# Kernel tuning notes

Hardware: AMD Instinct MI355X
Metric: run time of the kernel (lower is better)

Reference implementation:

```python
import jax, jax.numpy as jnp
import numpy as np

T, B, N, H, NT = 4096, 8, 256, 512, 5
W_SCALE = 0.02


def setup_inputs() -> dict:
    key = jax.random.key(0)
    ks = jax.random.split(key, 32)
    f32 = jnp.float32
    d = {}
    d['v_action'] = jax.random.normal(ks[0], (N, B, H), f32)
    d['v_frame'] = jax.random.normal(ks[1], (T, B, H), f32)
    d['v_task'] = jax.random.normal(ks[2], (NT, B, H), f32)
    d['v_mask'] = jax.random.randint(ks[3], (B, N), 0, 2, jnp.int32).at[:, 0].set(1)
    d['t_action'] = jax.random.normal(ks[4], (N, B, H), f32)
    d['t_frame'] = jax.random.normal(ks[5], (T, B, H), f32)
    d['t_task'] = jax.random.normal(ks[6], (NT, B, H), f32)
    d['t_mask'] = jax.random.randint(ks[7], (B, N), 0, 2, jnp.int32).at[:, 0].set(1)
    names = ['v_Wq', 'v_Wk', 'v_Wv', 'v_Wo', 't_Wq', 't_Wk', 't_Wv', 't_Wo']
    for i, nm in enumerate(names):
        d[nm] = jax.random.normal(ks[8 + i], (H, H), f32) * W_SCALE
    d['v_aw'] = jnp.asarray(0.1, f32)
    d['t_aw'] = jnp.asarray(0.1, f32)
    d['v_tw'] = jax.random.normal(ks[20], (H, 1), f32) * W_SCALE
    d['v_tb'] = jnp.zeros((1,), f32)
    d['t_tw'] = jax.random.normal(ks[21], (H, 1), f32) * W_SCALE
    d['t_tb'] = jnp.zeros((1,), f32)
    return d


def _compute_logit(frame, action, Wq, Wk):
    # frame: [T,B,H] queries, action: [N,B,H] keys -> logits [B,T,N]
    q = jnp.einsum('tbf,fh->tbh', frame, Wq)
    k = jnp.einsum('nba,ah->nbh', action, Wk)
    return jnp.einsum('tbh,nbh->btn', q, k) / jnp.sqrt(jnp.asarray(q.shape[-1], q.dtype))


def _compute_output(logit, alignment, action, frame, mask, Wv, Wo, aw):
    # shared detached cross-domain alignment, gated by sigmoid(alignment_weight)
    combined = logit + jax.nn.sigmoid(aw) * alignment          # [B,T,N]
    nomask = combined
    masked = jnp.where(mask[:, None, :] > 0, combined, -jnp.inf)
    attn = jax.nn.softmax(masked, axis=-1)                      # softmax over protos N
    v = jnp.einsum('nba,af->nbf', action, Wv)                   # values from protos
    out = jnp.einsum('btn,nbf->tbf', attn, v)
    out = jnp.einsum('tbf,fg->tbg', out, Wo) + frame            # residual to frames
    return out, nomask


def reference(v_action, v_frame, v_task, v_mask, t_action, t_frame, t_task, t_mask,
              v_Wq, v_Wk, v_Wv, v_Wo, v_aw, v_tw, v_tb,
              t_Wq, t_Wk, t_Wv, t_Wo, t_aw, t_tw, t_tb):
    v_logit = _compute_logit(v_frame, v_action, v_Wq, v_Wk)
    t_logit = _compute_logit(t_frame, t_action, t_Wq, t_Wk)
    v_share = jax.lax.stop_gradient(v_logit)
    t_share = jax.lax.stop_gradient(t_logit)
    v_out, v_nm = _compute_output(v_logit, t_share, v_action, v_frame, v_mask, v_Wv, v_Wo, v_aw)
    t_out, t_nm = _compute_output(t_logit, v_share, t_action, t_frame, t_mask, t_Wv, t_Wo, t_aw)
    v_ta = jnp.einsum('kbh,ho->kbo', v_task, v_tw) + v_tb       # [ntask,B,1]
    t_ta = jnp.einsum('kbh,ho->kbo', t_task, t_tw) + t_tb
    return (v_out, t_out,
            jnp.transpose(v_nm, (0, 2, 1)),                      # [B,N,T]
            jnp.transpose(t_nm, (0, 2, 1)),
            v_ta, t_ta)
```

## Files before the change

### kernel.cpp

```cpp
#include <hip/hip_runtime.h>
#include <hip/hip_bf16.h>
#include <cstddef>
#include <cstdint>

#define T_DIM 4096
#define B_DIM 8
#define N_DIM 256
#define H_DIM 512
#define NT_DIM 5

typedef __attribute__((ext_vector_type(8))) short short8;
typedef __attribute__((ext_vector_type(4))) float f32x4;

__device__ __forceinline__ short cvt_bf16(float f) {
  __hip_bfloat16 h = __float2bfloat16(f);
  union { __hip_bfloat16 h; short s; } u; u.h = h; return u.s;
}
__device__ __forceinline__ float bf2f(short s) {
  union { uint32_t u; float f; } v; v.u = ((uint32_t)(uint16_t)s) << 16;
  return v.f;
}

typedef __attribute__((address_space(1))) const void gvoid_t;
typedef __attribute__((address_space(3))) void lvoid_t;
__device__ __forceinline__ void gl_lds16(const void* g, void* lds_wave_base) {
  __builtin_amdgcn_global_load_lds((gvoid_t*)(uintptr_t)g,
                                   (lvoid_t*)(uint32_t)(uintptr_t)lds_wave_base,
                                   16, 0, 0);
}

#define MFMA16(a, b, c) __builtin_amdgcn_mfma_f32_16x16x32_bf16(a, b, c, 0, 0, 0)

struct GP {
  const void* A[4];
  const short* B[4];
  void* C[4];
  const float* R[4];
  long long a_bs[4], b_bs[4], c_bs[4];
  int lda[4], ldb[4], ldc[4];
  int xlim[4], ylim[4];
};

template<typename TA, typename TC, bool ADD_RES>
__global__ __launch_bounds__(256)
void gemm_tn(GP p, int zlog, int K, float scale) {
  constexpr bool F32A = (sizeof(TA) == 4);
  constexpr int ASTR = F32A ? 40 : 32;
  constexpr int AB = 128 * ASTR * 2;
  constexpr int BB = 128 * 32 * 2;
  constexpr int HALF = AB + BB;
  constexpr int EPIB = 4 * 16 * 68 * 4;
  constexpr int BODYB = F32A ? (2 * AB + 3 * BB) : (3 * HALF);
  constexpr int SMEMB = BODYB > EPIB ? BODYB : EPIB;
  __shared__ __align__(16) char smem[SMEMB];

  const int dom = blockIdx.z >> zlog;
  const long long zz = blockIdx.z & ((1u << zlog) - 1u);
  if ((int)blockIdx.x >= p.xlim[dom] || (int)blockIdx.y >= p.ylim[dom]) return;

  const int lda = p.lda[dom], ldb = p.ldb[dom], ldc = p.ldc[dom];

  const int tid  = threadIdx.x;
  const int lane = tid & 63;
  const int wave = tid >> 6;
  const int wr   = (wave >> 1) * 64;
  const int wc   = (wave & 1) * 64;
  const int lrow = lane & 15;
  const int kgrp = lane >> 4;

  const TA*    Abase = (const TA*)p.A[dom] + zz * p.a_bs[dom] +
                       (long long)(blockIdx.x * 128) * lda;
  const short* Bbase = p.B[dom] + zz * p.b_bs[dom] +
                       (long long)(blockIdx.y * 128) * ldb;

  const int ch_r  = lane >> 2;
  const int swcol = ((lane & 3) ^ (ch_r & 3)) * 8;
  const int srow = tid >> 1;
  const int scol = (tid & 1) * 16;

  f32x4 acc[4][4] = {};
  f32x4 pv[4];

  auto stageA_bf16 = [&](int buf, int k0) {
    short* As = (short*)(smem + buf * HALF);
    #pragma unroll
    for (int i = 0; i < 2; ++i) {
      const int c = wave + 4 * i;
      gl_lds16((const short*)Abase + (long long)(c * 16 + ch_r) * lda + k0 + swcol,
               &As[c * 512]);
    }
  };
  auto stageB_bf16 = [&](int buf, int k0) {
    short* Bs = (short*)(smem + buf * HALF + AB);
    #pragma unroll
    for (int i = 0; i < 2; ++i) {
      const int c = wave + 4 * i;
      gl_lds16(Bbase + (long long)(c * 16 + ch_r) * ldb + k0 + swcol, &Bs[c * 512]);
    }
  };
  auto stageB_f32p = [&](int buf, int k0) {
    short* Bs = (short*)(smem + 2 * AB + buf * BB);
    #pragma unroll
    for (int i = 0; i < 2; ++i) {
      const int c = wave + 4 * i;
      gl_lds16(Bbase + (long long)(c * 16 + ch_r) * ldb + k0 + swcol, &Bs[c * 512]);
    }
  };
  auto loadA_f32 = [&](int k0) {
    const float* gp = (const float*)Abase + (long long)srow * lda + k0 + scol;
    pv[0] = *(const f32x4*)(gp + 0);
    pv[1] = *(const f32x4*)(gp + 4);
    pv[2] = *(const f32x4*)(gp + 8);
    pv[3] = *(const f32x4*)(gp + 12);
  };
  auto writeA_f32 = [&](int buf) {
    short* As = (short*)(smem + buf * AB);
    short8 s0, s1;
    #pragma unroll
    for (int e = 0; e < 4; ++e) {
      s0[e]     = cvt_bf16(pv[0][e]);
      s0[4 + e] = cvt_bf16(pv[1][e]);
      s1[e]     = cvt_bf16(pv[2][e]);
      s1[4 + e] = cvt_bf16(pv[3][e]);
    }
    *(short8*)&As[srow * ASTR + scol]     = s0;
    *(short8*)&As[srow * ASTR + scol + 8] = s1;
  };
  auto compute = [&](int abuf, int bbuf) {
    const short* As = (const short*)(smem + (F32A ? abuf * AB : abuf * HALF));
    const short* Bs = (const short*)(smem + (F32A ? 2 * AB + bbuf * BB
                                                  : bbuf * HALF + AB));
    short8 af[4], bfr[4];
    const int u = kgrp ^ (lrow & 3);
    #pragma unroll
    for (int i = 0; i < 4; ++i) {
      const int row = wr + i * 16 + lrow;
      if constexpr (F32A) af[i] = *(const short8*)&As[row * ASTR + kgrp * 8];
      else                af[i] = *(const short8*)&As[row * 32 + u * 8];
    }
    #pragma unroll
    for (int j = 0; j < 4; ++j) {
      const int row = wc + j * 16 + lrow;
      bfr[j] = *(const short8*)&Bs[row * 32 + u * 8];
    }
    #pragma unroll
    for (int i = 0; i < 4; ++i)
      #pragma unroll
      for (int j = 0; j < 4; ++j)
        acc[i][j] = MFMA16(af[i], bfr[j], acc[i][j]);
  };

  const int NT = K >> 5;
  if constexpr (F32A) {
    loadA_f32(0); writeA_f32(0);
    stageB_f32p(0, 0);
    if (NT > 1) stageB_f32p(1, 32);
    if (NT > 1) loadA_f32(32);
    for (int t = 0; t < NT; ++t) {
      asm volatile("s_waitcnt lgkmcnt(0)" ::: "memory");
      __builtin_amdgcn_sched_barrier(0);
      __builtin_amdgcn_s_barrier();
      if (t + 2 < NT) stageB_f32p((t + 2) % 3, (t + 2) << 5);
      __builtin_amdgcn_sched_barrier(0);
      if (t + 2 < NT)      asm volatile("s_waitcnt vmcnt(8)" ::: "memory");
      else if (t + 1 < NT) asm volatile("s_waitcnt vmcnt(6)" ::: "memory");
      else                 asm volatile("s_waitcnt vmcnt(0)" ::: "memory");
      __builtin_amdgcn_sched_barrier(0);
      __builtin_amdgcn_s_barrier();
      __builtin_amdgcn_sched_barrier(0);
      compute(t & 1, t % 3);
      if (t + 1 < NT) writeA_f32((t + 1) & 1);
      if (t + 2 < NT) loadA_f32((t + 2) << 5);
    }
  } else {
    stageA_bf16(0, 0); stageB_bf16(0, 0);
    if (NT > 1) { stageA_bf16(1, 32); stageB_bf16(1, 32); }
    for (int t = 0; t < NT; ++t) {
      __builtin_amdgcn_s_barrier();
      if (t + 2 < NT) {
        stageA_bf16((t + 2) % 3, (t + 2) << 5);
        stageB_bf16((t + 2) % 3, (t + 2) << 5);
        __builtin_amdgcn_sched_barrier(0);
        asm volatile("s_waitcnt vmcnt(8)" ::: "memory");
      } else if (t + 1 < NT) {
        asm volatile("s_waitcnt vmcnt(4)" ::: "memory");
      } else {
        asm volatile("s_waitcnt vmcnt(0)" ::: "memory");
      }
      __builtin_amdgcn_sched_barrier(0);
      __builtin_amdgcn_s_barrier();
      __builtin_amdgcn_sched_barrier(0);
      compute(t % 3, t % 3);
    }
  }

  __syncthreads();
  float* myEp = (float*)smem + wave * (16 * 68);
  TC* Cd = (TC*)p.C[dom];
  const float* Res = p.R[dom];
  const long long cb = zz * p.c_bs[dom];
  const int gm = blockIdx.x * 128 + wr;
  const int gn = blockIdx.y * 128 + wc;
  const int er = lane >> 2;
  const int ec = (lane & 3) * 16;

  f32x4 resA[4], resB[4];
  if constexpr (ADD_RES) {
    const long long b0 = cb + (long long)(gm + er) * ldc + gn + ec;
    #pragma unroll
    for (int q = 0; q < 4; ++q) resA[q] = *(const f32x4*)&Res[b0 + q * 4];
  }

  #pragma unroll
  for (int i = 0; i < 4; ++i) {
    if constexpr (ADD_RES) {
      if (i < 3) {
        const long long bn = cb + (long long)(gm + (i + 1) * 16 + er) * ldc + gn + ec;
        #pragma unroll
        for (int q = 0; q < 4; ++q) resB[q] = *(const f32x4*)&Res[bn + q * 4];
      }
    }
    #pragma unroll
    for (int j = 0; j < 4; ++j)
      #pragma unroll
      for (int r = 0; r < 4; ++r)
        myEp[(kgrp * 4 + r) * 68 + j * 16 + lrow] = acc[i][j][r];
    float vals[16];
    #pragma unroll
    for (int q = 0; q < 4; ++q) {
      f32x4 t4 = *(const f32x4*)&myEp[er * 68 + ec + q * 4];
      vals[q * 4 + 0] = t4[0]; vals[q * 4 + 1] = t4[1];
      vals[q * 4 + 2] = t4[2]; vals[q * 4 + 3] = t4[3];
    }
    const int row_g = gm + i * 16 + er;
    const long long base = cb + (long long)row_g * ldc + gn + ec;
    if constexpr (sizeof(TC) == 2) {
      short8 s0, s1;
      #pragma unroll
      for (int e = 0; e < 8; ++e) {
        s0[e] = cvt_bf16(vals[e] * scale);
        s1[e] = cvt_bf16(vals[8 + e] * scale);
      }
      *(short8*)&Cd[base]     = s0;
      *(short8*)&Cd[base + 8] = s1;
    } else {
      #pragma unroll
      for (int q = 0; q < 4; ++q) {
        f32x4 o;
        #pragma unroll
        for (int e = 0; e < 4; ++e) o[e] = vals[q * 4 + e] * scale;
        if constexpr (ADD_RES) {
          #pragma unroll
          for (int e = 0; e < 4; ++e) o[e] += resA[q][e];
        }
        *(f32x4*)&Cd[base + q * 4] = o;
      }
    }
    if constexpr (ADD_RES) {
      #pragma unroll
      for (int q = 0; q < 4; ++q) resA[q] = resB[q];
    }
  }
}

struct PrepArgs {
  const float* w6[6];
  const float* w2[2];
  const float* av; const float* at;
  const float* vtask; const float* ttask;
  const float* vtw; const float* vtb;
  const float* ttw; const float* ttb;
  short* WT; short* Ac16v; short* Ac16t;
  float* out_vta; float* out_tta;
};

__global__ __launch_bounds__(256)
void prep_kernel(PrepArgs a) {
  __shared__ float tile[32][33];
  const long long WS = (long long)H_DIM * H_DIM;
  const int bx = blockIdx.x;
  const int tid = threadIdx.x;

  if (bx < 768) {
    const int w = bx >> 7;
    const int blk = bx & 127;
    const float* src = a.w6[w];
    short* d = a.WT + (long long)w * WS;
    const int i = (blk * 256 + tid) * 8;
    f32x4 v0 = *(const f32x4*)(src + i);
    f32x4 v1 = *(const f32x4*)(src + i + 4);
    short8 o;
    #pragma unroll
    for (int e = 0; e < 4; ++e) { o[e] = cvt_bf16(v0[e]); o[4 + e] = cvt_bf16(v1[e]); }
    *(short8*)&d[i] = o;
  } else if (bx < 1280) {
    const int r = bx - 768;
    const int w = r >> 8;
    const int rem = r & 255;
    const int n0 = (rem >> 4) * 32, k0 = (rem & 15) * 32;
    const float* src = a.w2[w];
    short* d = a.WT + (long long)(6 + w) * WS;
    const int tx = tid & 31, ty = tid >> 5;
    #pragma unroll
    for (int i = 0; i < 4; ++i)
      tile[ty + 8 * i][tx] = src[(long long)(k0 + ty + 8 * i) * H_DIM + n0 + tx];
    __syncthreads();
    #pragma unroll
    for (int i = 0; i < 4; ++i)
      d[(long long)(n0 + ty + 8 * i) * H_DIM + k0 + tx] = cvt_bf16(tile[tx][ty + 8 * i]);
  } else if (bx < 2304) {
    const int r = bx - 1280;
    const int dom = r >> 9;
    const int blk = r & 511;
    const float* src = dom ? a.at : a.av;
    short* d = dom ? a.Ac16t : a.Ac16v;
    const int i = (blk * 256 + tid) * 8;
    f32x4 v0 = *(const f32x4*)(src + i);
    f32x4 v1 = *(const f32x4*)(src + i + 4);
    short8 o;
    #pragma unroll
    for (int e = 0; e < 4; ++e) { o[e] = cvt_bf16(v0[e]); o[4 + e] = cvt_bf16(v1[e]); }
    *(short8*)&d[i] = o;
  } else {
    const int wave = tid >> 6;
    const int lane = tid & 63;
    for (int g = wave; g < 16; g += 4) {
      const int dom = g >> 3;
      const int b = g & 7;
      const float* task = dom ? a.ttask : a.vtask;
      const float* tw   = dom ? a.ttw : a.vtw;
      const float  tb   = (dom ? a.ttb : a.vtb)[0];
      float* o = dom ? a.out_tta : a.out_vta;
      for (int k = 0; k < NT_DIM; ++k) {
        const float* row = task + ((long long)k * B_DIM + b) * H_DIM;
        float s = 0.f;
        for (int c = lane; c < H_DIM; c += 64) s += row[c] * tw[c];
        #pragma unroll
        for (int d = 32; d > 0; d >>= 1) s += __shfl_xor(s, d);
        if (lane == 0) o[k * B_DIM + b] = s + tb;
      }
    }
  }
}

__global__ __launch_bounds__(256)
void softmax_fused(const short* __restrict__ Lv, const short* __restrict__ Lt,
                   const int* __restrict__ vmask, const int* __restrict__ tmask,
                   const float* __restrict__ vaw, const float* __restrict__ taw,
                   short* __restrict__ Av, short* __restrict__ At,
                   float* __restrict__ Onm_v, float* __restrict__ Onm_t) {
  __shared__ float tile[16 * 260];
  __shared__ int msk[2][256];
  const int tid = threadIdx.x;
  const int b = blockIdx.y, t0 = blockIdx.x * 16;
  const int r = tid >> 4, seg = tid & 15;
  msk[0][tid] = vmask[b * 256 + tid];
  msk[1][tid] = tmask[b * 256 + tid];
  __syncthreads();
  const float sv = 1.f / (1.f + __expf(-vaw[0]));
  const float st = 1.f / (1.f + __expf(-taw[0]));
  const long long off = ((long long)b * T_DIM + t0 + r) * N_DIM + seg * 16;

  short8 lv0 = *(const short8*)&Lv[off];
  short8 lv1 = *(const short8*)&Lv[off + 8];
  short8 lt0 = *(const short8*)&Lt[off];
  short8 lt1 = *(const short8*)&Lt[off + 8];
  float cv[16], ct[16];
  #pragma unroll
  for (int i = 0; i < 8; ++i) {
    float a0 = bf2f(lv0[i]), b0 = bf2f(lt0[i]);
    float a1 = bf2f(lv1[i]), b1 = bf2f(lt1[i]);
    cv[i]     = a0 + sv * b0;  ct[i]     = b0 + st * a0;
    cv[8 + i] = a1 + sv * b1;  ct[8 + i] = b1 + st * a1;
  }

#define EMIT_DOMAIN(CVAL, DI, AOUT, ONM) do {                                   \
    const int4 mA = *(const int4*)&msk[DI][seg * 16 + 0];                       \
    const int4 mB = *(const int4*)&msk[DI][seg * 16 + 4];                       \
    const int4 mC = *(const int4*)&msk[DI][seg * 16 + 8];                       \
    const int4 mD = *(const int4*)&msk[DI][seg * 16 + 12];                      \
    const int mk[16] = {mA.x, mA.y, mA.z, mA.w, mB.x, mB.y, mB.z, mB.w,         \
                        mC.x, mC.y, mC.z, mC.w, mD.x, mD.y, mD.z, mD.w};        \
    float mx = -3.4e38f;                                                        \
    _Pragma("unroll")                                                           \
    for (int q = 0; q < 16; ++q) if (mk[q] > 0) mx = fmaxf(mx, CVAL[q]);        \
    _Pragma("unroll")                                                           \
    for (int sh = 1; sh < 16; sh <<= 1) mx = fmaxf(mx, __shfl_xor(mx, sh));     \
    float ev[16]; float ssum = 0.f;                                             \
    _Pragma("unroll")                                                           \
    for (int q = 0; q < 16; ++q) {                                              \
      ev[q] = (mk[q] > 0) ? __expf(CVAL[q] - mx) : 0.f; ssum += ev[q];          \
    }                                                                           \
    _Pragma("unroll")                                                           \
    for (int sh = 1; sh < 16; sh <<= 1) ssum += __shfl_xor(ssum, sh);           \
    const float inv = 1.f / ssum;                                               \
    short8 o0, o1;                                                              \
    _Pragma("unroll")                                                           \
    for (int q = 0; q < 8; ++q) {                                               \
      o0[q] = cvt_bf16(ev[q] * inv); o1[q] = cvt_bf16(ev[8 + q] * inv);         \
    }                                                                           \
    *(short8*)&AOUT[off] = o0; *(short8*)&AOUT[off + 8] = o1;                   \
    _Pragma("unroll")                                                           \
    for (int q = 0; q < 4; ++q) {                                               \
      f32x4 tv; tv[0] = CVAL[q * 4]; tv[1] = CVAL[q * 4 + 1];                   \
      tv[2] = CVAL[q * 4 + 2]; tv[3] = CVAL[q * 4 + 3];                         \
      *(f32x4*)&tile[r * 260 + seg * 16 + q * 4] = tv;                          \
    }                                                                           \
    __syncthreads();                                                            \
    {                                                                           \
      float* obase = &ONM[((long long)b * N_DIM + tid) * T_DIM + t0];           \
      _Pragma("unroll")                                                         \
      for (int g = 0; g < 4; ++g) {                                             \
        f32x4 wv;                                                               \
        wv[0] = tile[(4 * g + 0) * 260 + tid];                                  \
        wv[1] = tile[(4 * g + 1) * 260 + tid];                                  \
        wv[2] = tile[(4 * g + 2) * 260 + tid];                                  \
        wv[3] = tile[(4 * g + 3) * 260 + tid];                                  \
        *(f32x4*)&obase[4 * g] = wv;                                            \
      }                                                                         \
    }                                                                           \
    __syncthreads();                                                            \
  } while (0)

  EMIT_DOMAIN(cv, 0, Av, Onm_v);
  EMIT_DOMAIN(ct, 1, At, Onm_t);
#undef EMIT_DOMAIN
}

extern "C" void kernel_launch(void* const* d_in, const int* in_sizes, int n_in,
                              void* d_out, int out_size, void* d_ws, size_t ws_size,
                              hipStream_t stream) {
  const float* v_action = (const float*)d_in[0];
  const float* v_frame  = (const float*)d_in[1];
  const float* v_task   = (const float*)d_in[2];
  const int*   v_mask   = (const int*)d_in[3];
  const float* t_action = (const float*)d_in[4];
  const float* t_frame  = (const float*)d_in[5];
  const float* t_task   = (const float*)d_in[6];
  const int*   t_mask   = (const int*)d_in[7];
  const float* v_aw = (const float*)d_in[16];
  const float* t_aw = (const float*)d_in[17];
  const float* v_tw = (const float*)d_in[18];
  const float* v_tb = (const float*)d_in[19];
  const float* t_tw = (const float*)d_in[20];
  const float* t_tb = (const float*)d_in[21];

  const long long TBH = (long long)T_DIM * B_DIM * H_DIM;
  const long long BTN = (long long)B_DIM * T_DIM * N_DIM;
  const long long WS  = (long long)H_DIM * H_DIM;

  float* out = (float*)d_out;
  float* out_v   = out;
  float* out_t   = out + TBH;
  float* out_vnm = out + 2 * TBH;
  float* out_tnm = out + 2 * TBH + BTN;
  float* out_vta = out + 2 * TBH + 2 * BTN;
  float* out_tta = out_vta + NT_DIM * B_DIM;

  char* w = (char*)d_ws;
  auto alloc = [&](long long bytes) {
    char* p = w; w += (bytes + 255) & ~255LL; return p;
  };
  short* WT    = (short*)alloc(8 * WS * 2);
  short* Mv    = (short*)alloc(WS * 2);
  short* Mt    = (short*)alloc(WS * 2);
  short* PTv   = (short*)alloc(WS * 2);
  short* PTt   = (short*)alloc(WS * 2);
  short* Ac16v = (short*)alloc(1048576LL * 2);
  short* Ac16t = (short*)alloc(1048576LL * 2);
  short* KWTv  = (short*)alloc(8LL * 131072 * 2);
  short* KWTt  = (short*)alloc(8LL * 131072 * 2);
  short* VWTv  = (short*)alloc(8LL * 131072 * 2);
  short* VWTt  = (short*)alloc(8LL * 131072 * 2);
  short* Av    = (short*)alloc(BTN * 2);
  short* At    = (short*)alloc(BTN * 2);
  short* Lv    = (short*)alloc(BTN * 2);
  short* Lt    = (short*)alloc(BTN * 2);

  const float rsq = 0.044194173824159216f;

  {
    PrepArgs a;
    a.w6[0] = (const float*)d_in[8];  a.w6[1] = (const float*)d_in[9];
    a.w6[2] = (const float*)d_in[10]; a.w6[3] = (const float*)d_in[12];
    a.w6[4] = (const float*)d_in[13]; a.w6[5] = (const float*)d_in[14];
    a.w2[0] = (const float*)d_in[11]; a.w2[1] = (const float*)d_in[15];
    a.av = v_action; a.at = t_action;
    a.vtask = v_task; a.ttask = t_task;
    a.vtw = v_tw; a.vtb = v_tb; a.ttw = t_tw; a.ttb = t_tb;
    a.WT = WT; a.Ac16v = Ac16v; a.Ac16t = Ac16t;
    a.out_vta = out_vta; a.out_tta = out_tta;
    prep_kernel<<<dim3(2305), dim3(256), 0, stream>>>(a);
  }

  {
    GP p = {};
    const short* As[4] = {WT + 0 * WS, WT + 3 * WS, WT + 6 * WS, WT + 7 * WS};
    const short* Bs[4] = {WT + 1 * WS, WT + 4 * WS, WT + 2 * WS, WT + 5 * WS};
    short* Cs[4] = {Mv, Mt, PTv, PTt};
    for (int s = 0; s < 4; ++s) {
      p.A[s] = As[s]; p.B[s] = Bs[s]; p.C[s] = Cs[s]; p.R[s] = nullptr;
      p.a_bs[s] = 0; p.b_bs[s] = 0; p.c_bs[s] = 0;
      p.lda[s] = H_DIM; p.ldb[s] = H_DIM; p.ldc[s] = H_DIM;
      p.xlim[s] = 4; p.ylim[s] = 4;
    }
    gemm_tn<short, short, false><<<dim3(4, 4, 4), dim3(256), 0, stream>>>(
        p, 0, 512, 1.f);
  }

  {
    GP p = {};
    p.A[0] = Ac16v; p.B[0] = Mv; p.C[0] = KWTv;
    p.A[1] = Ac16t; p.B[1] = Mt; p.C[1] = KWTt;
    for (int s = 0; s < 2; ++s) {
      p.a_bs[s] = 512; p.lda[s] = B_DIM * H_DIM;
      p.b_bs[s] = 0;   p.ldb[s] = H_DIM;
      p.c_bs[s] = 131072; p.ldc[s] = H_DIM;
      p.xlim[s] = 2; p.ylim[s] = 4; p.R[s] = nullptr;
    }
    p.A[2] = PTv; p.B[2] = Ac16v; p.C[2] = VWTv;
    p.A[3] = PTt; p.B[3] = Ac16t; p.C[3] = VWTt;
    for (int s = 2; s < 4; ++s) {
      p.a_bs[s] = 0;   p.lda[s] = H_DIM;
      p.b_bs[s] = 512; p.ldb[s] = B_DIM * H_DIM;
      p.c_bs[s] = 131072; p.ldc[s] = N_DIM;
      p.xlim[s] = 4; p.ylim[s] = 2; p.R[s] = nullptr;
    }
    gemm_tn<short, short, false><<<dim3(4, 4, 32), dim3(256), 0, stream>>>(
        p, 3, 512, 1.f);
  }

  {
    GP p = {};
    p.A[0] = v_frame; p.B[0] = KWTv; p.C[0] = Lv;
    p.A[1] = t_frame; p.B[1] = KWTt; p.C[1] = Lt;
    for (int s = 0; s < 2; ++s) {
      p.a_bs[s] = 512; p.lda[s] = B_DIM * H_DIM;
      p.b_bs[s] = 131072; p.ldb[s] = H_DIM;
      p.c_bs[s] = (long long)T_DIM * N_DIM; p.ldc[s] = N_DIM;
      p.xlim[s] = 32; p.ylim[s] = 2; p.R[s] = nullptr;
    }
    gemm_tn<float, short, false><<<dim3(32, 2, 16), dim3(256), 0, stream>>>(
        p, 3, 512, rsq);
  }

  softmax_fused<<<dim3(T_DIM / 16, B_DIM), dim3(256), 0, stream>>>(
      Lv, Lt, v_mask, t_mask, v_aw, t_aw, Av, At, out_vnm, out_tnm);

  {
    GP p = {};
    p.A[0] = Av; p.B[0] = VWTv; p.C[0] = out_v; p.R[0] = v_frame;
    p.A[1] = At; p.B[1] = VWTt; p.C[1] = out_t; p.R[1] = t_frame;
    for (int s = 0; s < 2; ++s) {
      p.a_bs[s] = (long long)T_DIM * N_DIM; p.lda[s] = N_DIM;
      p.b_bs[s] = 131072; p.ldb[s] = N_DIM;
      p.c_bs[s] = 512; p.ldc[s] = B_DIM * H_DIM;
      p.xlim[s] = 32; p.ylim[s] = 4;
    }
    gemm_tn<short, float, true><<<dim3(32, 4, 16), dim3(256), 0, stream>>>(
        p, 3, 256, 1.f);
  }
}
```

Measured before the change: 277.7 us.

## Pre-convert frames to bf16 and use a flat, XCD-swizzled grid for big GEMMs

```diff
diff --git a/kernel.cpp b/kernel.cpp
--- a/kernel.cpp
+++ b/kernel.cpp
@@ -32,33 +32,39 @@
 #define MFMA16(a, b, c) __builtin_amdgcn_mfma_f32_16x16x32_bf16(a, b, c, 0, 0, 0)
 
 struct GP {
-  const void* A[4];
+  const short* A[4];
   const short* B[4];
   void* C[4];
-  const float* R[4];
-  long long a_bs[4], b_bs[4], c_bs[4];
-  int lda[4], ldb[4], ldc[4];
-  int xlim[4], ylim[4];
+  const short* R[4];
 };
 
-template<typename TA, typename TC, bool ADD_RES>
+template<typename TC, bool ADD_RES, bool FLAT = false>
 __global__ __launch_bounds__(256)
-void gemm_tn(GP p, int zlog, int K, float scale) {
-  constexpr bool F32A = (sizeof(TA) == 4);
-  constexpr int ASTR = F32A ? 40 : 32;
-  constexpr int AB = 128 * ASTR * 2;
+void gemm_tn(GP p, int zlog, long long a_bs, int lda,
+             long long b_bs, int ldb, long long c_bs, int ldc,
+             int K, float scale, int NX = 1, int NY = 1) {
+  constexpr int AB = 128 * 32 * 2;
   constexpr int BB = 128 * 32 * 2;
   constexpr int HALF = AB + BB;
   constexpr int EPIB = 4 * 16 * 68 * 4;
-  constexpr int BODYB = F32A ? (2 * AB + 3 * BB) : (3 * HALF);
+  constexpr int BODYB = 3 * HALF;
   constexpr int SMEMB = BODYB > EPIB ? BODYB : EPIB;
   __shared__ __align__(16) char smem[SMEMB];
 
-  const int dom = blockIdx.z >> zlog;
-  const long long zz = blockIdx.z & ((1u << zlog) - 1u);
-  if ((int)blockIdx.x >= p.xlim[dom] || (int)blockIdx.y >= p.ylim[dom]) return;
-
-  const int lda = p.lda[dom], ldb = p.ldb[dom], ldc = p.ldc[dom];
+  int bx, by, zidx;
+  if constexpr (FLAT) {
+    const int q = gridDim.x >> 3;
+    const int lid = (blockIdx.x & 7) * q + (blockIdx.x >> 3);
+    zidx = lid / (NX * NY);
+    const int rem = lid - zidx * (NX * NY);
+    bx = rem / NY;
+    by = rem - bx * NY;
+  } else {
+    bx = blockIdx.x; by = blockIdx.y; zidx = blockIdx.z;
+  }
+
+  const int dom = zidx >> zlog;
+  const long long zz = zidx & ((1u << zlog) - 1u);
 
   const int tid  = threadIdx.x;
   const int lane = tid & 63;
@@ -68,29 +74,23 @@
   const int lrow = lane & 15;
   const int kgrp = lane >> 4;
 
-  const TA*    Abase = (const TA*)p.A[dom] + zz * p.a_bs[dom] +
-                       (long long)(blockIdx.x * 128) * lda;
-  const short* Bbase = p.B[dom] + zz * p.b_bs[dom] +
-                       (long long)(blockIdx.y * 128) * ldb;
+  const short* Abase = p.A[dom] + zz * a_bs + (long long)(bx * 128) * lda;
+  const short* Bbase = p.B[dom] + zz * b_bs + (long long)(by * 128) * ldb;
 
   const int ch_r  = lane >> 2;
   const int swcol = ((lane & 3) ^ (ch_r & 3)) * 8;
-  const int srow = tid >> 1;
-  const int scol = (tid & 1) * 16;
 
   f32x4 acc[4][4] = {};
-  f32x4 pv[4];
-
-  auto stageA_bf16 = [&](int buf, int k0) {
+
+  auto stageA = [&](int buf, int k0) {
     short* As = (short*)(smem + buf * HALF);
     #pragma unroll
     for (int i = 0; i < 2; ++i) {
       const int c = wave + 4 * i;
-      gl_lds16((const short*)Abase + (long long)(c * 16 + ch_r) * lda + k0 + swcol,
-               &As[c * 512]);
+      gl_lds16(Abase + (long long)(c * 16 + ch_r) * lda + k0 + swcol, &As[c * 512]);
     }
   };
-  auto stageB_bf16 = [&](int buf, int k0) {
+  auto stageB = [&](int buf, int k0) {
     short* Bs = (short*)(smem + buf * HALF + AB);
     #pragma unroll
     for (int i = 0; i < 2; ++i) {
@@ -98,45 +98,15 @@
       gl_lds16(Bbase + (long long)(c * 16 + ch_r) * ldb + k0 + swcol, &Bs[c * 512]);
     }
   };
-  auto stageB_f32p = [&](int buf, int k0) {
-    short* Bs = (short*)(smem + 2 * AB + buf * BB);
-    #pragma unroll
-    for (int i = 0; i < 2; ++i) {
-      const int c = wave + 4 * i;
-      gl_lds16(Bbase + (long long)(c * 16 + ch_r) * ldb + k0 + swcol, &Bs[c * 512]);
-    }
-  };
-  auto loadA_f32 = [&](int k0) {
-    const float* gp = (const float*)Abase + (long long)srow * lda + k0 + scol;
-    pv[0] = *(const f32x4*)(gp + 0);
-    pv[1] = *(const f32x4*)(gp + 4);
-    pv[2] = *(const f32x4*)(gp + 8);
-    pv[3] = *(const f32x4*)(gp + 12);
-  };
-  auto writeA_f32 = [&](int buf) {
-    short* As = (short*)(smem + buf * AB);
-    short8 s0, s1;
-    #pragma unroll
-    for (int e = 0; e < 4; ++e) {
-      s0[e]     = cvt_bf16(pv[0][e]);
-      s0[4 + e] = cvt_bf16(pv[1][e]);
-      s1[e]     = cvt_bf16(pv[2][e]);
-      s1[4 + e] = cvt_bf16(pv[3][e]);
-    }
-    *(short8*)&As[srow * ASTR + scol]     = s0;
-    *(short8*)&As[srow * ASTR + scol + 8] = s1;
-  };
-  auto compute = [&](int abuf, int bbuf) {
-    const short* As = (const short*)(smem + (F32A ? abuf * AB : abuf * HALF));
-    const short* Bs = (const short*)(smem + (F32A ? 2 * AB + bbuf * BB
-                                                  : bbuf * HALF + AB));
+  auto compute = [&](int buf) {
+    const short* As = (const short*)(smem + buf * HALF);
+    const short* Bs = (const short*)(smem + buf * HALF + AB);
     short8 af[4], bfr[4];
     const int u = kgrp ^ (lrow & 3);
     #pragma unroll
     for (int i = 0; i < 4; ++i) {
       const int row = wr + i * 16 + lrow;
-      if constexpr (F32A) af[i] = *(const short8*)&As[row * ASTR + kgrp * 8];
-      else                af[i] = *(const short8*)&As[row * 32 + u * 8];
+      af[i] = *(const short8*)&As[row * 32 + u * 8];
     }
     #pragma unroll
     for (int j = 0; j < 4; ++j) {
@@ -151,64 +121,41 @@
   };
 
   const int NT = K >> 5;
-  if constexpr (F32A) {
-    loadA_f32(0); writeA_f32(0);
-    stageB_f32p(0, 0);
-    if (NT > 1) stageB_f32p(1, 32);
-    if (NT > 1) loadA_f32(32);
-    for (int t = 0; t < NT; ++t) {
-      asm volatile("s_waitcnt lgkmcnt(0)" ::: "memory");
+  stageA(0, 0); stageB(0, 0);
+  if (NT > 1) { stageA(1, 32); stageB(1, 32); }
+  for (int t = 0; t < NT; ++t) {
+    __builtin_amdgcn_s_barrier();
+    if (t + 2 < NT) {
+      stageA((t + 2) % 3, (t + 2) << 5);
+      stageB((t + 2) % 3, (t + 2) << 5);
       __builtin_amdgcn_sched_barrier(0);
-      __builtin_amdgcn_s_barrier();
-      if (t + 2 < NT) stageB_f32p((t + 2) % 3, (t + 2) << 5);
-      __builtin_amdgcn_sched_barrier(0);
-      if (t + 2 < NT)      asm volatile("s_waitcnt vmcnt(8)" ::: "memory");
-      else if (t + 1 < NT) asm volatile("s_waitcnt vmcnt(6)" ::: "memory");
-      else                 asm volatile("s_waitcnt vmcnt(0)" ::: "memory");
-      __builtin_amdgcn_sched_barrier(0);
-      __builtin_amdgcn_s_barrier();
-      __builtin_amdgcn_sched_barrier(0);
-      compute(t & 1, t % 3);
-      if (t + 1 < NT) writeA_f32((t + 1) & 1);
-      if (t + 2 < NT) loadA_f32((t + 2) << 5);
-    }
-  } else {
-    stageA_bf16(0, 0); stageB_bf16(0, 0);
-    if (NT > 1) { stageA_bf16(1, 32); stageB_bf16(1, 32); }
-    for (int t = 0; t < NT; ++t) {
-      __builtin_amdgcn_s_barrier();
-      if (t + 2 < NT) {
-        stageA_bf16((t + 2) % 3, (t + 2) << 5);
-        stageB_bf16((t + 2) % 3, (t + 2) << 5);
-        __builtin_amdgcn_sched_barrier(0);
-        asm volatile("s_waitcnt vmcnt(8)" ::: "memory");
-      } else if (t + 1 < NT) {
-        asm volatile("s_waitcnt vmcnt(4)" ::: "memory");
-      } else {
-        asm volatile("s_waitcnt vmcnt(0)" ::: "memory");
-      }
-      __builtin_amdgcn_sched_barrier(0);
-      __builtin_amdgcn_s_barrier();
-      __builtin_amdgcn_sched_barrier(0);
-      compute(t % 3, t % 3);
-    }
+      asm volatile("s_waitcnt vmcnt(8)" ::: "memory");
+    } else if (t + 1 < NT) {
+      asm volatile("s_waitcnt vmcnt(4)" ::: "memory");
+    } else {
+      asm volatile("s_waitcnt vmcnt(0)" ::: "memory");
+    }
+    __builtin_amdgcn_sched_barrier(0);
+    __builtin_amdgcn_s_barrier();
+    __builtin_amdgcn_sched_barrier(0);
+    compute(t % 3);
   }
 
   __syncthreads();
   float* myEp = (float*)smem + wave * (16 * 68);
   TC* Cd = (TC*)p.C[dom];
-  const float* Res = p.R[dom];
-  const long long cb = zz * p.c_bs[dom];
-  const int gm = blockIdx.x * 128 + wr;
-  const int gn = blockIdx.y * 128 + wc;
+  const short* Res = p.R[dom];
+  const long long cb = zz * c_bs;
+  const int gm = bx * 128 + wr;
+  const int gn = by * 128 + wc;
   const int er = lane >> 2;
   const int ec = (lane & 3) * 16;
 
-  f32x4 resA[4], resB[4];
+  short8 rA0, rA1, rB0, rB1;
   if constexpr (ADD_RES) {
     const long long b0 = cb + (long long)(gm + er) * ldc + gn + ec;
-    #pragma unroll
-    for (int q = 0; q < 4; ++q) resA[q] = *(const f32x4*)&Res[b0 + q * 4];
+    rA0 = *(const short8*)&Res[b0];
+    rA1 = *(const short8*)&Res[b0 + 8];
   }
 
   #pragma unroll
@@ -216,8 +163,8 @@
     if constexpr (ADD_RES) {
       if (i < 3) {
         const long long bn = cb + (long long)(gm + (i + 1) * 16 + er) * ldc + gn + ec;
-        #pragma unroll
-        for (int q = 0; q < 4; ++q) resB[q] = *(const f32x4*)&Res[bn + q * 4];
+        rB0 = *(const short8*)&Res[bn];
+        rB1 = *(const short8*)&Res[bn + 8];
       }
     }
     #pragma unroll
@@ -248,18 +195,18 @@
       for (int q = 0; q < 4; ++q) {
         f32x4 o;
         #pragma unroll
-        for (int e = 0; e < 4; ++e) o[e] = vals[q * 4 + e] * scale;
-        if constexpr (ADD_RES) {
-          #pragma unroll
-          for (int e = 0; e < 4; ++e) o[e] += resA[q][e];
+        for (int e = 0; e < 4; ++e) {
+          float v = vals[q * 4 + e] * scale;
+          if constexpr (ADD_RES) {
+            const int col = q * 4 + e;
+            v += bf2f(col < 8 ? rA0[col & 7] : rA1[col & 7]);
+          }
+          o[e] = v;
         }
         *(f32x4*)&Cd[base + q * 4] = o;
       }
     }
-    if constexpr (ADD_RES) {
-      #pragma unroll
-      for (int q = 0; q < 4; ++q) resA[q] = resB[q];
-    }
+    if constexpr (ADD_RES) { rA0 = rB0; rA1 = rB1; }
   }
 }
 
@@ -267,10 +214,12 @@
   const float* w6[6];
   const float* w2[2];
   const float* av; const float* at;
+  const float* fv; const float* ft;
   const float* vtask; const float* ttask;
   const float* vtw; const float* vtb;
   const float* ttw; const float* ttb;
   short* WT; short* Ac16v; short* Ac16t;
+  short* Fr16v; short* Fr16t;
   float* out_vta; float* out_tta;
 };
 
@@ -315,6 +264,19 @@
     const float* src = dom ? a.at : a.av;
     short* d = dom ? a.Ac16t : a.Ac16v;
     const int i = (blk * 256 + tid) * 8;
+    f32x4 v0 = *(const f32x4*)(src + i);
+    f32x4 v1 = *(const f32x4*)(src + i + 4);
+    short8 o;
+    #pragma unroll
+    for (int e = 0; e < 4; ++e) { o[e] = cvt_bf16(v0[e]); o[4 + e] = cvt_bf16(v1[e]); }
+    *(short8*)&d[i] = o;
+  } else if (bx < 18688) {
+    const int r = bx - 2304;
+    const int dom = r >> 13;
+    const int blk = r & 8191;
+    const float* src = dom ? a.ft : a.fv;
+    short* d = dom ? a.Fr16t : a.Fr16v;
+    const long long i = ((long long)blk * 256 + tid) * 8;
     f32x4 v0 = *(const f32x4*)(src + i);
     f32x4 v1 = *(const f32x4*)(src + i + 4);
     short8 o;
@@ -336,7 +298,7 @@
         float s = 0.f;
         for (int c = lane; c < H_DIM; c += 64) s += row[c] * tw[c];
         #pragma unroll
-        for (int d = 32; d > 0; d >>= 1) s += __shfl_xor(s, d);
+        for (int d2 = 32; d2 > 0; d2 >>= 1) s += __shfl_xor(s, d2);
         if (lane == 0) o[k * B_DIM + b] = s + tb;
       }
     }
@@ -468,6 +430,8 @@
   short* PTt   = (short*)alloc(WS * 2);
   short* Ac16v = (short*)alloc(1048576LL * 2);
   short* Ac16t = (short*)alloc(1048576LL * 2);
+  short* Fr16v = (short*)alloc(TBH * 2);
+  short* Fr16t = (short*)alloc(TBH * 2);
   short* KWTv  = (short*)alloc(8LL * 131072 * 2);
   short* KWTt  = (short*)alloc(8LL * 131072 * 2);
   short* VWTv  = (short*)alloc(8LL * 131072 * 2);
@@ -486,78 +450,50 @@
     a.w6[4] = (const float*)d_in[13]; a.w6[5] = (const float*)d_in[14];
     a.w2[0] = (const float*)d_in[11]; a.w2[1] = (const float*)d_in[15];
     a.av = v_action; a.at = t_action;
+    a.fv = v_frame;  a.ft = t_frame;
     a.vtask = v_task; a.ttask = t_task;
     a.vtw = v_tw; a.vtb = v_tb; a.ttw = t_tw; a.ttb = t_tb;
     a.WT = WT; a.Ac16v = Ac16v; a.Ac16t = Ac16t;
+    a.Fr16v = Fr16v; a.Fr16t = Fr16t;
     a.out_vta = out_vta; a.out_tta = out_tta;
-    prep_kernel<<<dim3(2305), dim3(256), 0, stream>>>(a);
-  }
-
-  {
-    GP p = {};
-    const short* As[4] = {WT + 0 * WS, WT + 3 * WS, WT + 6 * WS, WT + 7 * WS};
-    const short* Bs[4] = {WT + 1 * WS, WT + 4 * WS, WT + 2 * WS, WT + 5 * WS};
-    short* Cs[4] = {Mv, Mt, PTv, PTt};
-    for (int s = 0; s < 4; ++s) {
-      p.A[s] = As[s]; p.B[s] = Bs[s]; p.C[s] = Cs[s]; p.R[s] = nullptr;
-      p.a_bs[s] = 0; p.b_bs[s] = 0; p.c_bs[s] = 0;
-      p.lda[s] = H_DIM; p.ldb[s] = H_DIM; p.ldc[s] = H_DIM;
-      p.xlim[s] = 4; p.ylim[s] = 4;
-    }
-    gemm_tn<short, short, false><<<dim3(4, 4, 4), dim3(256), 0, stream>>>(
-        p, 0, 512, 1.f);
-  }
-
-  {
-    GP p = {};
-    p.A[0] = Ac16v; p.B[0] = Mv; p.C[0] = KWTv;
-    p.A[1] = Ac16t; p.B[1] = Mt; p.C[1] = KWTt;
-    for (int s = 0; s < 2; ++s) {
-      p.a_bs[s] = 512; p.lda[s] = B_DIM * H_DIM;
-      p.b_bs[s] = 0;   p.ldb[s] = H_DIM;
-      p.c_bs[s] = 131072; p.ldc[s] = H_DIM;
-      p.xlim[s] = 2; p.ylim[s] = 4; p.R[s] = nullptr;
-    }
-    p.A[2] = PTv; p.B[2] = Ac16v; p.C[2] = VWTv;
-    p.A[3] = PTt; p.B[3] = Ac16t; p.C[3] = VWTt;
-    for (int s = 2; s < 4; ++s) {
-      p.a_bs[s] = 0;   p.lda[s] = H_DIM;
-      p.b_bs[s] = 512; p.ldb[s] = B_DIM * H_DIM;
-      p.c_bs[s] = 131072; p.ldc[s] = N_DIM;
-      p.xlim[s] = 4; p.ylim[s] = 2; p.R[s] = nullptr;
-    }
-    gemm_tn<short, short, false><<<dim3(4, 4, 32), dim3(256), 0, stream>>>(
-        p, 3, 512, 1.f);
-  }
-
-  {
-    GP p = {};
-    p.A[0] = v_frame; p.B[0] = KWTv; p.C[0] = Lv;
-    p.A[1] = t_frame; p.B[1] = KWTt; p.C[1] = Lt;
-    for (int s = 0; s < 2; ++s) {
-      p.a_bs[s] = 512; p.lda[s] = B_DIM * H_DIM;
-      p.b_bs[s] = 131072; p.ldb[s] = H_DIM;
-      p.c_bs[s] = (long long)T_DIM * N_DIM; p.ldc[s] = N_DIM;
-      p.xlim[s] = 32; p.ylim[s] = 2; p.R[s] = nullptr;
-    }
-    gemm_tn<float, short, false><<<dim3(32, 2, 16), dim3(256), 0, stream>>>(
-        p, 3, 512, rsq);
+    prep_kernel<<<dim3(18689), dim3(256), 0, stream>>>(a);
+  }
+
+  {
+    GP p = {{WT + 0 * WS, WT + 3 * WS, WT + 6 * WS, WT + 7 * WS},
+            {WT + 1 * WS, WT + 4 * WS, WT + 2 * WS, WT + 5 * WS},
+            {Mv, Mt, PTv, PTt},
+            {nullptr, nullptr, nullptr, nullptr}};
+    gemm_tn<short, false><<<dim3(4, 4, 4), dim3(256), 0, stream>>>(
+        p, 0, 0LL, H_DIM, 0LL, H_DIM, 0LL, H_DIM, 512, 1.f);
+  }
+
+  {
+    GP p = {{Ac16v, Ac16t}, {Mv, Mt}, {KWTv, KWTt}, {nullptr, nullptr}};
+    gemm_tn<short, false><<<dim3(2, 4, 16), dim3(256), 0, stream>>>(
+        p, 3, 512LL, B_DIM * H_DIM, 0LL, H_DIM, 131072LL, H_DIM, 512, 1.f);
+  }
+
+  {
+    GP p = {{PTv, PTt}, {Ac16v, Ac16t}, {VWTv, VWTt}, {nullptr, nullptr}};
+    gemm_tn<short, false><<<dim3(4, 2, 16), dim3(256), 0, stream>>>(
+        p, 3, 0LL, H_DIM, 512LL, B_DIM * H_DIM, 131072LL, N_DIM, 512, 1.f);
+  }
+
+  {
+    GP p = {{Fr16v, Fr16t}, {KWTv, KWTt}, {Lv, Lt}, {nullptr, nullptr}};
+    gemm_tn<short, false, true><<<dim3(32 * 2 * 16), dim3(256), 0, stream>>>(
+        p, 3, 512LL, B_DIM * H_DIM, 131072LL, H_DIM,
+        (long long)T_DIM * N_DIM, N_DIM, 512, rsq, 32, 2);
   }
 
   softmax_fused<<<dim3(T_DIM / 16, B_DIM), dim3(256), 0, stream>>>(
       Lv, Lt, v_mask, t_mask, v_aw, t_aw, Av, At, out_vnm, out_tnm);
 
   {
-    GP p = {};
-    p.A[0] = Av; p.B[0] = VWTv; p.C[0] = out_v; p.R[0] = v_frame;
-    p.A[1] = At; p.B[1] = VWTt; p.C[1] = out_t; p.R[1] = t_frame;
-    for (int s = 0; s < 2; ++s) {
-      p.a_bs[s] = (long long)T_DIM * N_DIM; p.lda[s] = N_DIM;
-      p.b_bs[s] = 131072; p.ldb[s] = N_DIM;
-      p.c_bs[s] = 512; p.ldc[s] = B_DIM * H_DIM;
-      p.xlim[s] = 32; p.ylim[s] = 4;
-    }
-    gemm_tn<short, float, true><<<dim3(32, 4, 16), dim3(256), 0, stream>>>(
-        p, 3, 256, 1.f);
-  }
-}
+    GP p = {{Av, At}, {VWTv, VWTt}, {out_v, out_t}, {Fr16v, Fr16t}};
+    gemm_tn<float, true, true><<<dim3(32 * 4 * 16), dim3(256), 0, stream>>>(
+        p, 3, (long long)T_DIM * N_DIM, N_DIM, 131072LL, N_DIM,
+        512LL, B_DIM * H_DIM, 256, 1.f, 32, 4);
+  }
+}
```

Result: slower. 285.4 us (+2.8%).
